# Kernel optimization log

Measured on AMD Instinct MI355X. Metric: run time of the kernel, lower is better.

Reference implementation:

```python
import jax, jax.numpy as jnp
import numpy as np

N = 16384      # nodes (radar cells x batched graphs)
H = 128        # n_hidden
N_ENV = 7
N_IN = N_ENV + 2 + 1  # env + coords + density = 10
T_CTX = 24
HORIZON = 40
T = T_CTX + HORIZON


def setup_inputs() -> dict:
    key = jax.random.key(0)
    ks = jax.random.split(key, 40)

    def w(k, shape, fan_in):
        return jax.random.normal(k, shape, jnp.float32) * np.float32(1.0 / np.sqrt(fan_in))

    inp = {}
    inp["x"] = jax.random.normal(ks[0], (N, T), jnp.float32)
    inp["coords"] = jax.random.normal(ks[1], (N, 2), jnp.float32)
    inp["env"] = jax.random.normal(ks[2], (N, N_ENV, T), jnp.float32)
    # --- encoder params ---
    inp["enc_W_in"] = w(ks[3], (H, N_IN), N_IN)           # Linear(n_in->H), no bias
    inp["enc_Wih0"] = w(ks[4], (4 * H, H), H)
    inp["enc_Whh0"] = w(ks[5], (4 * H, H), H)
    inp["enc_bih0"] = jnp.zeros((4 * H,), jnp.float32)
    inp["enc_bhh0"] = jnp.zeros((4 * H,), jnp.float32)
    inp["enc_Wih1"] = w(ks[6], (4 * H, H), H)
    inp["enc_Whh1"] = w(ks[7], (4 * H, H), H)
    inp["enc_bih1"] = jnp.zeros((4 * H,), jnp.float32)
    inp["enc_bhh1"] = jnp.zeros((4 * H,), jnp.float32)
    # --- NodeLSTM params ---
    inp["node_W_in"] = w(ks[8], (H, N_IN), N_IN)          # Linear(n_in->H), no bias
    inp["in_Wih"] = w(ks[9], (4 * H, 2 * H), 2 * H)       # lstm_in takes [inputs, enc_state]
    inp["in_Whh"] = w(ks[10], (4 * H, H), H)
    inp["in_bih"] = jnp.zeros((4 * H,), jnp.float32)
    inp["in_bhh"] = jnp.zeros((4 * H,), jnp.float32)
    inp["l1_Wih"] = w(ks[11], (4 * H, H), H)
    inp["l1_Whh"] = w(ks[12], (4 * H, H), H)
    inp["l1_bih"] = jnp.zeros((4 * H,), jnp.float32)
    inp["l1_bhh"] = jnp.zeros((4 * H,), jnp.float32)
    # hidden2in / hidden2out heads: Linear(H,H) -> ReLU -> Linear(H,1)
    inp["h2in_W1"] = w(ks[13], (H, H), H)
    inp["h2in_b1"] = jnp.zeros((H,), jnp.float32)
    inp["h2in_W2"] = w(ks[14], (1, H), H)
    inp["h2in_b2"] = jnp.zeros((1,), jnp.float32)
    inp["h2out_W1"] = w(ks[15], (H, H), H)
    inp["h2out_b1"] = jnp.zeros((H,), jnp.float32)
    inp["h2out_W2"] = w(ks[16], (1, H), H)
    inp["h2out_b2"] = jnp.zeros((1,), jnp.float32)
    return inp


def _lstm_cell(xin, h, c, Wih, Whh, bih, bhh):
    # torch.nn.LSTMCell semantics; gate order i, f, g, o
    gates = xin @ Wih.T + h @ Whh.T + (bih + bhh)
    i, f, g, o = jnp.split(gates, 4, axis=1)
    c_new = jax.nn.sigmoid(f) * c + jax.nn.sigmoid(i) * jnp.tanh(g)
    h_new = jax.nn.sigmoid(o) * jnp.tanh(c_new)
    return h_new, c_new


def reference(x, coords, env,
              enc_W_in, enc_Wih0, enc_Whh0, enc_bih0, enc_bhh0,
              enc_Wih1, enc_Whh1, enc_bih1, enc_bhh1,
              node_W_in, in_Wih, in_Whh, in_bih, in_bhh,
              l1_Wih, l1_Whh, l1_bih, l1_bhh,
              h2in_W1, h2in_b1, h2in_W2, h2in_b2,
              h2out_W1, h2out_b1, h2out_W2, h2out_b2):
    n = x.shape[0]
    z = jnp.zeros((n, H), x.dtype)

    # ---------- encoder: scan over T_CTX context steps ----------
    def enc_step(carry, xs):
        h0, c0, h1, c1 = carry
        xt, et = xs  # [N], [N, N_ENV]
        inp = jnp.concatenate([xt[:, None], coords, et], axis=1) @ enc_W_in.T
        h0, c0 = _lstm_cell(inp, h0, c0, enc_Wih0, enc_Whh0, enc_bih0, enc_bhh0)
        h1, c1 = _lstm_cell(h0, h1, c1, enc_Wih1, enc_Whh1, enc_bih1, enc_bhh1)
        return (h0, c0, h1, c1), None

    enc_xs = (x[:, :T_CTX].T, jnp.moveaxis(env[:, :, :T_CTX], 2, 0))
    (h0, c0, h1, c1), _ = jax.lax.scan(enc_step, (z, z, z, z), enc_xs)
    enc_state = h1  # h[-1] captured at setup_states, fixed over the horizon

    def head(hid, W1, b1, W2, b2):
        return jax.nn.sigmoid(jax.nn.relu(hid @ W1.T + b1) @ W2.T + b2)

    # ---------- decoder: scan over HORIZON forecast steps ----------
    def dec_step(carry, et):
        xc, h0, c0, h1, c1 = carry
        inp = jnp.concatenate([xc, coords, et], axis=1) @ node_W_in.T
        inp = jnp.concatenate([inp, enc_state], axis=1)  # [N, 2H]
        h0, c0 = _lstm_cell(inp, h0, c0, in_Wih, in_Whh, in_bih, in_bhh)
        h1, c1 = _lstm_cell(h0, h1, c1, l1_Wih, l1_Whh, l1_bih, l1_bhh)
        x_in = head(h1, h2in_W1, h2in_b1, h2in_W2, h2in_b2)
        x_out = head(h1, h2out_W1, h2out_b1, h2out_W2, h2out_b2)
        xn = xc + x_in - x_out * xc  # source/sink update, [N, 1]
        return (xn, h0, c0, h1, c1), xn

    x0 = x[:, T_CTX - 1][:, None]
    dec_xs = jnp.moveaxis(env[:, :, T_CTX:T_CTX + HORIZON], 2, 0)
    _, ys = jax.lax.scan(dec_step, (x0, h0, c0, h1, c1), dec_xs)  # [HORIZON, N, 1]
    return jnp.transpose(ys[..., 0], (1, 0))  # [N, HORIZON]
```

## Files before the change

kernel.cpp:

```cpp
#include <hip/hip_runtime.h>
#include <hip/hip_bf16.h>
#include <cstdint>
#include <cstddef>

typedef __bf16 bf16_t;
typedef bf16_t bf16x8 __attribute__((ext_vector_type(8)));
typedef bf16_t bf16x4 __attribute__((ext_vector_type(4)));
typedef float  f32x4  __attribute__((ext_vector_type(4)));

#define TT    64
#define T_CTX 24
#define HOR   40
#define ST    136
#define NTH   512

#define MFMA __builtin_amdgcn_mfma_f32_16x16x32_bf16

#define O_WIH0   16
#define O_WHH0   (O_WIH0  + 65536)
#define O_WIH1   (O_WHH0  + 65536)
#define O_WHH1   (O_WIH1  + 65536)
#define O_INWIH  (O_WHH1  + 65536)
#define O_INWHH  (O_INWIH + 131072)
#define O_L1WIH  (O_INWHH + 65536)
#define O_L1WHH  (O_L1WIH + 65536)
#define O_HIW1   (O_L1WHH + 65536)
#define O_HOW1   (O_HIW1  + 16384)
#define O_BIAS   (O_HOW1  + 16384)
#define O_HEADP  (O_BIAS  + 2048)
#define O_WINE   (O_HEADP + 512)
#define O_WINN   (O_WINE  + 1536)
#define O_B2     (O_WINN  + 1536)

struct Ptrs { const void* q[29]; };

__device__ __forceinline__ float sigm(float x) {
  return __builtin_amdgcn_rcpf(1.f + __expf(-x));
}
__device__ __forceinline__ float tanh_(float x) {
  return 1.f - 2.f * __builtin_amdgcn_rcpf(1.f + __expf(2.f * x));
}
__device__ __forceinline__ unsigned pk2(float a, float b) {
  unsigned ua = __float_as_uint(a), ub = __float_as_uint(b);
  ua = (ua + 0x7fffu + ((ua >> 16) & 1u)) >> 16;
  ub = (ub + 0x7fffu + ((ub >> 16) & 1u)) >> 16;
  return ua | (ub << 16);
}
__device__ __forceinline__ float uplo(unsigned p){ return __uint_as_float(p << 16); }
__device__ __forceinline__ float uphi(unsigned p){ return __uint_as_float(p & 0xffff0000u); }

__global__ void detect_kernel(const unsigned short* __restrict__ wsrc, int* __restrict__ flag)
{
  int tid = threadIdx.x;
  int wild = 0;
  for (int i = tid; i < 256; i += 64) {
    unsigned short b = wsrc[i];
    float v  = __uint_as_float(((unsigned)b) << 16);
    float av = fabsf(v);
    unsigned e = (b >> 7) & 0xff;
    if (av > 1000.f || e == 0xff || (((b & 0x7fff) != 0) && av < 1e-9f)) wild++;
  }
  for (int off = 32; off; off >>= 1) wild += __shfl_down(wild, off, 64);
  if (tid == 0) flag[0] = (wild > 16) ? 1 : 0;
}

__global__ void prep_kernel(Ptrs P, bf16_t* __restrict__ w, const int* __restrict__ flag)
{
  const bool f32 = (flag[0] != 0);
  const int gtid = blockIdx.x * blockDim.x + threadIdx.x;
  const int gsz  = gridDim.x * blockDim.x;

  auto rd = [&](const void* src, int i) -> float {
    return f32 ? ((const float*)src)[i] : (float)((const bf16_t*)src)[i];
  };
  auto cp = [&](const void* src, int dst, int n) {
    if (f32) { const float*  s = (const float*)src;
      for (int i = gtid; i < n; i += gsz) w[dst + i] = (bf16_t)s[i];
    } else   { const bf16_t* s = (const bf16_t*)src;
      for (int i = gtid; i < n; i += gsz) w[dst + i] = s[i];
    }
  };

  cp(P.q[4],  O_WIH0,  65536);
  cp(P.q[5],  O_WHH0,  65536);
  cp(P.q[8],  O_WIH1,  65536);
  cp(P.q[9],  O_WHH1,  65536);
  cp(P.q[13], O_INWIH, 131072);
  cp(P.q[14], O_INWHH, 65536);
  cp(P.q[17], O_L1WIH, 65536);
  cp(P.q[18], O_L1WHH, 65536);
  cp(P.q[21], O_HIW1,  16384);
  cp(P.q[25], O_HOW1,  16384);

  for (int i = gtid; i < 512; i += gsz) {
    w[O_BIAS + i]        = (bf16_t)(rd(P.q[6],  i) + rd(P.q[7],  i));
    w[O_BIAS + 512 + i]  = (bf16_t)(rd(P.q[10], i) + rd(P.q[11], i));
    w[O_BIAS + 1024 + i] = (bf16_t)(rd(P.q[15], i) + rd(P.q[16], i));
    w[O_BIAS + 1536 + i] = (bf16_t)(rd(P.q[19], i) + rd(P.q[20], i));
  }
  for (int i = gtid; i < 128; i += gsz) {
    w[O_HEADP + i]       = (bf16_t)rd(P.q[22], i);
    w[O_HEADP + 128 + i] = (bf16_t)rd(P.q[23], i);
    w[O_HEADP + 256 + i] = (bf16_t)rd(P.q[26], i);
    w[O_HEADP + 384 + i] = (bf16_t)rd(P.q[27], i);
  }
  for (int i = gtid; i < 1536; i += gsz) {
    int cc = i / 12, j = i % 12;
    w[O_WINE + i] = (j < 10) ? (bf16_t)rd(P.q[3],  cc * 10 + j) : (bf16_t)0.f;
    w[O_WINN + i] = (j < 10) ? (bf16_t)rd(P.q[12], cc * 10 + j) : (bf16_t)0.f;
  }
  if (gtid == 0) {
    w[O_B2]     = (bf16_t)rd(P.q[24], 0);
    w[O_B2 + 1] = (bf16_t)rd(P.q[28], 0);
  }
}

template<int NKT>
__device__ __forceinline__ void gemm_bt(f32x4 (&acc)[4][4], const bf16_t* __restrict__ As,
                                        const bf16_t* __restrict__ W, int rs, int kofs,
                                        int wid, int l, int q)
{
#pragma unroll
  for (int kt = 0; kt < NKT; ++kt) {
    const int k0 = kt * 32 + q * 8;
    bf16x8 a0 = *(const bf16x8*)(As + (0 * 16 + l) * ST + k0);
    bf16x8 a1 = *(const bf16x8*)(As + (1 * 16 + l) * ST + k0);
    bf16x8 a2 = *(const bf16x8*)(As + (2 * 16 + l) * ST + k0);
    bf16x8 a3 = *(const bf16x8*)(As + (3 * 16 + l) * ST + k0);
#pragma unroll
    for (int g = 0; g < 4; ++g) {
      bf16x8 b = *(const bf16x8*)(W + (size_t)(g * 128 + wid * 16 + l) * rs + kofs + k0);
      acc[g][0] = MFMA(a0, b, acc[g][0], 0, 0, 0);
      acc[g][1] = MFMA(a1, b, acc[g][1], 0, 0, 0);
      acc[g][2] = MFMA(a2, b, acc[g][2], 0, 0, 0);
      acc[g][3] = MFMA(a3, b, acc[g][3], 0, 0, 0);
    }
  }
}

__device__ __forceinline__ void cell_update(f32x4 (&acc)[4][4], float (&c)[16],
                                            bf16_t* __restrict__ sh,
                                            const bf16_t* __restrict__ bias,
                                            int wid, int l, int q)
{
  const int jc = wid * 16 + l;
  const float bi  = (float)bias[jc];
  const float bf_ = (float)bias[128 + jc];
  const float bg  = (float)bias[256 + jc];
  const float bo  = (float)bias[384 + jc];
#pragma unroll
  for (int mt = 0; mt < 4; ++mt) {
#pragma unroll
    for (int r = 0; r < 4; ++r) {
      float gi = acc[0][mt][r] + bi;
      float gf = acc[1][mt][r] + bf_;
      float gg = acc[2][mt][r] + bg;
      float go = acc[3][mt][r] + bo;
      float cn = sigm(gf) * c[mt * 4 + r] + sigm(gi) * tanh_(gg);
      float hh = sigm(go) * tanh_(cn);
      c[mt * 4 + r] = cn;
      sh[(mt * 16 + q * 4 + r) * ST + jc] = (bf16_t)hh;
    }
  }
}

__device__ __forceinline__ void proj16(const float* v, const bf16_t* __restrict__ wbase,
                                       bf16_t* __restrict__ sx, int nd, int sub)
{
  bf16x8 o0, o1;
#pragma unroll
  for (int cc = 0; cc < 16; ++cc) {
    const bf16_t* wr = wbase + (sub * 16 + cc) * 12;
    bf16x4 w0 = *(const bf16x4*)(wr);
    bf16x4 w1 = *(const bf16x4*)(wr + 4);
    bf16x4 w2 = *(const bf16x4*)(wr + 8);
    float a = v[0] * (float)w0[0] + v[1] * (float)w0[1] + v[2] * (float)w0[2] + v[3] * (float)w0[3]
            + v[4] * (float)w1[0] + v[5] * (float)w1[1] + v[6] * (float)w1[2] + v[7] * (float)w1[3]
            + v[8] * (float)w2[0] + v[9] * (float)w2[1];
    if (cc < 8) o0[cc] = (bf16_t)a; else o1[cc - 8] = (bf16_t)a;
  }
  *(bf16x8*)(sx + nd * ST + sub * 16)     = o0;
  *(bf16x8*)(sx + nd * ST + sub * 16 + 8) = o1;
}

template<typename T>
__global__ __launch_bounds__(NTH, 2) void lstm_persist(
    const T* __restrict__ x, const T* __restrict__ coords, const T* __restrict__ env,
    const bf16_t* __restrict__ w, const int* __restrict__ flag, T* __restrict__ out)
{
  const bool want_f32 = (sizeof(T) == 4);
  if ((flag[0] != 0) != want_f32) return;

  __shared__ __align__(16) bf16_t s_x [64 * ST];
  __shared__ __align__(16) bf16_t s_h0[64 * ST];
  __shared__ __align__(16) bf16_t s_h1[64 * ST];
  __shared__ __align__(16) bf16_t s_win[2 * 128 * 12];
  __shared__ __align__(16) bf16_t s_bias[4 * 512];
  __shared__ float s_red[128];
  __shared__ float s_xc[64];

  const int tid = threadIdx.x;
  const int wid = tid >> 6;
  const int l   = tid & 15;
  const int q   = (tid & 63) >> 4;
  const int node0 = blockIdx.x * 64;
  const int nd  = tid >> 3;
  const int sub = tid & 7;

  for (int i = tid; i < 2048; i += NTH) s_bias[i] = w[O_BIAS + i];
  for (int i = tid; i < 3072; i += NTH) s_win[i]  = w[O_WINE + i];
  for (int i = tid; i < 64 * ST; i += NTH) { s_h0[i] = (bf16_t)0.f; s_h1[i] = (bf16_t)0.f; }

  const float cx = (float)coords[(size_t)(node0 + nd) * 2 + 0];
  const float cy = (float)coords[(size_t)(node0 + nd) * 2 + 1];

  float c0[16], c1[16];
#pragma unroll
  for (int i = 0; i < 16; ++i) { c0[i] = 0.f; c1[i] = 0.f; }

  __syncthreads();

#pragma unroll 1
  for (int t = 0; t < T_CTX; ++t) {
    float v[10];
    v[0] = (float)x[(size_t)(node0 + nd) * TT + t];
    v[1] = cx; v[2] = cy;
#pragma unroll
    for (int e = 0; e < 7; ++e)
      v[3 + e] = (float)env[((size_t)(node0 + nd) * 7 + e) * TT + t];
    proj16(v, s_win, s_x, nd, sub);
    __syncthreads();

    f32x4 acc[4][4];
#pragma unroll
    for (int g = 0; g < 4; ++g)
#pragma unroll
      for (int mt = 0; mt < 4; ++mt) acc[g][mt] = f32x4{0.f, 0.f, 0.f, 0.f};
    gemm_bt<4>(acc, s_x,  w + O_WIH0, 128, 0, wid, l, q);
    gemm_bt<4>(acc, s_h0, w + O_WHH0, 128, 0, wid, l, q);
    __syncthreads();
    cell_update(acc, c0, s_h0, s_bias, wid, l, q);
    __syncthreads();

#pragma unroll
    for (int g = 0; g < 4; ++g)
#pragma unroll
      for (int mt = 0; mt < 4; ++mt) acc[g][mt] = f32x4{0.f, 0.f, 0.f, 0.f};
    gemm_bt<4>(acc, s_h0, w + O_WIH1, 128, 0, wid, l, q);
    gemm_bt<4>(acc, s_h1, w + O_WHH1, 128, 0, wid, l, q);
    __syncthreads();
    cell_update(acc, c1, s_h1, s_bias + 512, wid, l, q);
  }
  __syncthreads();

  uint2 geh[4][4], gel[4][4];
  {
    f32x4 acc[4][4];
#pragma unroll
    for (int g = 0; g < 4; ++g)
#pragma unroll
      for (int mt = 0; mt < 4; ++mt) acc[g][mt] = f32x4{0.f, 0.f, 0.f, 0.f};
    gemm_bt<4>(acc, s_h1, w + O_INWIH, 256, 128, wid, l, q);
#pragma unroll
    for (int g = 0; g < 4; ++g)
#pragma unroll
      for (int mt = 0; mt < 4; ++mt) {
        unsigned hx = pk2(acc[g][mt][0], acc[g][mt][1]);
        unsigned hy = pk2(acc[g][mt][2], acc[g][mt][3]);
        geh[g][mt] = uint2{hx, hy};
        gel[g][mt] = uint2{pk2(acc[g][mt][0] - uplo(hx), acc[g][mt][1] - uphi(hx)),
                           pk2(acc[g][mt][2] - uplo(hy), acc[g][mt][3] - uphi(hy))};
      }
  }
  if (tid < 64) s_xc[tid] = (float)x[(size_t)(node0 + tid) * TT + (T_CTX - 1)];
  const float b2i = (float)w[O_B2];
  const float b2o = (float)w[O_B2 + 1];
  const float b1i = (float)w[O_HEADP + wid * 16 + l];
  const float w2i = (float)w[O_HEADP + 128 + wid * 16 + l];
  const float b1o = (float)w[O_HEADP + 256 + wid * 16 + l];
  const float w2o = (float)w[O_HEADP + 384 + wid * 16 + l];
  __syncthreads();

#pragma unroll 1
  for (int s = 0; s < HOR; ++s) {
    const int t = T_CTX + s;
    float v[10];
    v[0] = s_xc[nd];
    v[1] = cx; v[2] = cy;
#pragma unroll
    for (int e = 0; e < 7; ++e)
      v[3 + e] = (float)env[((size_t)(node0 + nd) * 7 + e) * TT + t];
    proj16(v, s_win + 1536, s_x, nd, sub);
    __syncthreads();

    f32x4 acc[4][4];
#pragma unroll
    for (int g = 0; g < 4; ++g)
#pragma unroll
      for (int mt = 0; mt < 4; ++mt)
        acc[g][mt] = f32x4{uplo(geh[g][mt].x) + uplo(gel[g][mt].x),
                           uphi(geh[g][mt].x) + uphi(gel[g][mt].x),
                           uplo(geh[g][mt].y) + uplo(gel[g][mt].y),
                           uphi(geh[g][mt].y) + uphi(gel[g][mt].y)};
    gemm_bt<4>(acc, s_x,  w + O_INWIH, 256, 0, wid, l, q);
    gemm_bt<4>(acc, s_h0, w + O_INWHH, 128, 0, wid, l, q);
    __syncthreads();
    cell_update(acc, c0, s_h0, s_bias + 1024, wid, l, q);
    __syncthreads();

#pragma unroll
    for (int g = 0; g < 4; ++g)
#pragma unroll
      for (int mt = 0; mt < 4; ++mt) acc[g][mt] = f32x4{0.f, 0.f, 0.f, 0.f};
    gemm_bt<4>(acc, s_h0, w + O_L1WIH, 128, 0, wid, l, q);
    gemm_bt<4>(acc, s_h1, w + O_L1WHH, 128, 0, wid, l, q);
    __syncthreads();
    cell_update(acc, c1, s_h1, s_bias + 1536, wid, l, q);
    if (tid < 128) s_red[tid] = 0.f;
    __syncthreads();

    f32x4 hacc[2][4];
#pragma unroll
    for (int hd = 0; hd < 2; ++hd)
#pragma unroll
      for (int mt = 0; mt < 4; ++mt) hacc[hd][mt] = f32x4{0.f, 0.f, 0.f, 0.f};
#pragma unroll
    for (int kt = 0; kt < 4; ++kt) {
      const int k0 = kt * 32 + q * 8;
      bf16x8 a0 = *(const bf16x8*)(s_h1 + (0 * 16 + l) * ST + k0);
      bf16x8 a1 = *(const bf16x8*)(s_h1 + (1 * 16 + l) * ST + k0);
      bf16x8 a2 = *(const bf16x8*)(s_h1 + (2 * 16 + l) * ST + k0);
      bf16x8 a3 = *(const bf16x8*)(s_h1 + (3 * 16 + l) * ST + k0);
      bf16x8 bi_ = *(const bf16x8*)(w + O_HIW1 + (size_t)(wid * 16 + l) * 128 + k0);
      bf16x8 bo_ = *(const bf16x8*)(w + O_HOW1 + (size_t)(wid * 16 + l) * 128 + k0);
      hacc[0][0] = MFMA(a0, bi_, hacc[0][0], 0, 0, 0);
      hacc[0][1] = MFMA(a1, bi_, hacc[0][1], 0, 0, 0);
      hacc[0][2] = MFMA(a2, bi_, hacc[0][2], 0, 0, 0);
      hacc[0][3] = MFMA(a3, bi_, hacc[0][3], 0, 0, 0);
      hacc[1][0] = MFMA(a0, bo_, hacc[1][0], 0, 0, 0);
      hacc[1][1] = MFMA(a1, bo_, hacc[1][1], 0, 0, 0);
      hacc[1][2] = MFMA(a2, bo_, hacc[1][2], 0, 0, 0);
      hacc[1][3] = MFMA(a3, bo_, hacc[1][3], 0, 0, 0);
    }
#pragma unroll
    for (int hd = 0; hd < 2; ++hd) {
      const float b1v = hd ? b1o : b1i;
      const float w2v = hd ? w2o : w2i;
#pragma unroll
      for (int mt = 0; mt < 4; ++mt)
#pragma unroll
        for (int r = 0; r < 4; ++r) {
          float val = fmaxf(hacc[hd][mt][r] + b1v, 0.f) * w2v;
          val += __shfl_xor(val, 1, 64);
          val += __shfl_xor(val, 2, 64);
          val += __shfl_xor(val, 4, 64);
          val += __shfl_xor(val, 8, 64);
          if (l == 0) atomicAdd(&s_red[hd * 64 + mt * 16 + q * 4 + r], val);
        }
    }
    __syncthreads();
    if (tid < 64) {
      float xc = s_xc[tid];
      float si = sigm(s_red[tid] + b2i);
      float so = sigm(s_red[64 + tid] + b2o);
      float xn = xc + si - so * xc;
      s_xc[tid] = xn;
      out[(size_t)(node0 + tid) * HOR + s] = (T)xn;
    }
    __syncthreads();
  }
}

extern "C" void kernel_launch(void* const* d_in, const int* in_sizes, int n_in,
                              void* d_out, int out_size, void* d_ws, size_t ws_size,
                              hipStream_t stream) {
  (void)in_sizes; (void)n_in; (void)out_size; (void)ws_size;
  Ptrs P;
  for (int i = 0; i < 29; ++i) P.q[i] = d_in[i];
  int*    flag = (int*)d_ws;
  bf16_t* w    = (bf16_t*)d_ws;

  detect_kernel<<<1, 64, 0, stream>>>((const unsigned short*)d_in[4], flag);
  prep_kernel<<<256, 256, 0, stream>>>(P, w, flag);
  lstm_persist<float><<<256, NTH, 0, stream>>>(
      (const float*)d_in[0], (const float*)d_in[1], (const float*)d_in[2],
      w, flag, (float*)d_out);
  lstm_persist<bf16_t><<<256, NTH, 0, stream>>>(
      (const bf16_t*)d_in[0], (const bf16_t*)d_in[1], (const bf16_t*)d_in[2],
      w, flag, (bf16_t*)d_out);
}
```

Baseline: 2.216 ms.

## Pre-pack LSTM weights into MFMA fragment order and fuse input/hidden GEMMs

Weights are repacked in the prep kernel into per-wave, per-lane MFMA B-fragment order, so each lane reads a contiguous 16-byte chunk instead of strided rows. Activations [x|h] are now stored side by side in a 256-wide shared buffer, so each LSTM gate GEMM becomes one K=256 pass. The first B fragments of the next GEMM are prefetched before the barrier, and B loads within a GEMM use a three-slot rotating buffer. The constant encoder-state projection is now kept in a single bf16 copy instead of a hi/lo split, which gives up some precision in exchange for fewer registers. Register pressure goes up because of the prefetched fragments.

```diff
diff --git a/kernel.cpp b/kernel.cpp
--- a/kernel.cpp
+++ b/kernel.cpp
@@ -11,26 +11,19 @@
 #define TT    64
 #define T_CTX 24
 #define HOR   40
-#define ST    136
+#define SA    264
 #define NTH   512
 
 #define MFMA __builtin_amdgcn_mfma_f32_16x16x32_bf16
 
-#define O_WIH0   16
-#define O_WHH0   (O_WIH0  + 65536)
-#define O_WIH1   (O_WHH0  + 65536)
-#define O_WHH1   (O_WIH1  + 65536)
-#define O_INWIH  (O_WHH1  + 65536)
-#define O_INWHH  (O_INWIH + 131072)
-#define O_L1WIH  (O_INWHH + 65536)
-#define O_L1WHH  (O_L1WIH + 65536)
-#define O_HIW1   (O_L1WHH + 65536)
-#define O_HOW1   (O_HIW1  + 16384)
-#define O_BIAS   (O_HOW1  + 16384)
-#define O_HEADP  (O_BIAS  + 2048)
-#define O_WINE   (O_HEADP + 512)
-#define O_WINN   (O_WINE  + 1536)
-#define O_B2     (O_WINN  + 1536)
+#define O_PKE   16
+#define O_PKD   (O_PKE + 262144)
+#define O_PKX   (O_PKD + 294912)
+#define O_BIAS  (O_PKX + 131072)
+#define O_HEADP (O_BIAS + 2048)
+#define O_WINE  (O_HEADP + 512)
+#define O_WINN  (O_WINE + 1536)
+#define O_B2    (O_WINN + 1536)
 
 struct Ptrs { const void* q[29]; };
 
@@ -64,84 +57,123 @@
   if (tid == 0) flag[0] = (wild > 16) ? 1 : 0;
 }
 
-__global__ void prep_kernel(Ptrs P, bf16_t* __restrict__ w, const int* __restrict__ flag)
+__global__ void prep_kernel(Ptrs P, bf16_t* __restrict__ wb, const int* __restrict__ flag)
 {
   const bool f32 = (flag[0] != 0);
   const int gtid = blockIdx.x * blockDim.x + threadIdx.x;
   const int gsz  = gridDim.x * blockDim.x;
-
   auto rd = [&](const void* src, int i) -> float {
     return f32 ? ((const float*)src)[i] : (float)((const bf16_t*)src)[i];
   };
-  auto cp = [&](const void* src, int dst, int n) {
-    if (f32) { const float*  s = (const float*)src;
-      for (int i = gtid; i < n; i += gsz) w[dst + i] = (bf16_t)s[i];
-    } else   { const bf16_t* s = (const bf16_t*)src;
-      for (int i = gtid; i < n; i += gsz) w[dst + i] = s[i];
-    }
-  };
-
-  cp(P.q[4],  O_WIH0,  65536);
-  cp(P.q[5],  O_WHH0,  65536);
-  cp(P.q[8],  O_WIH1,  65536);
-  cp(P.q[9],  O_WHH1,  65536);
-  cp(P.q[13], O_INWIH, 131072);
-  cp(P.q[14], O_INWHH, 65536);
-  cp(P.q[17], O_L1WIH, 65536);
-  cp(P.q[18], O_L1WHH, 65536);
-  cp(P.q[21], O_HIW1,  16384);
-  cp(P.q[25], O_HOW1,  16384);
-
+
+  for (int i = gtid; i < 262144; i += gsz) {
+    int w = i >> 15, r = i & 32767, f = r >> 9, e = r & 511;
+    int ln = e >> 3, j = e & 7;
+    int seg = f >> 5, fk = f & 31, kt = fk >> 2, g = fk & 3;
+    int row = g * 128 + w * 16 + (ln & 15);
+    int col = kt * 32 + ((ln >> 4) << 3) + j;
+    float v;
+    if (seg == 0) v = (col < 128) ? rd(P.q[4], row * 128 + col) : rd(P.q[5], row * 128 + col - 128);
+    else          v = (col < 128) ? rd(P.q[8], row * 128 + col) : rd(P.q[9], row * 128 + col - 128);
+    wb[O_PKE + i] = (bf16_t)v;
+  }
+  for (int i = gtid; i < 294912; i += gsz) {
+    int w = i / 36864, r = i - w * 36864, f = r >> 9, e = r & 511;
+    int ln = e >> 3, j = e & 7;
+    int colk = ((ln >> 4) << 3) + j;
+    float v;
+    if (f < 64) {
+      int seg = f >> 5, fk = f & 31, kt = fk >> 2, g = fk & 3;
+      int row = g * 128 + w * 16 + (ln & 15);
+      int col = kt * 32 + colk;
+      if (seg == 0) v = (col < 128) ? rd(P.q[13], row * 256 + col) : rd(P.q[14], row * 128 + col - 128);
+      else          v = (col < 128) ? rd(P.q[17], row * 128 + col) : rd(P.q[18], row * 128 + col - 128);
+    } else {
+      int f2 = f - 64, h = f2 >> 2, kt = f2 & 3;
+      int row = w * 16 + (ln & 15);
+      int col = kt * 32 + colk;
+      v = rd(h ? P.q[25] : P.q[21], row * 128 + col);
+    }
+    wb[O_PKD + i] = (bf16_t)v;
+  }
+  for (int i = gtid; i < 131072; i += gsz) {
+    int w = i >> 14, r = i & 16383, f = r >> 9, e = r & 511;
+    int ln = e >> 3, j = e & 7;
+    int kt = f >> 2, g = f & 3;
+    int row = g * 128 + w * 16 + (ln & 15);
+    int col = kt * 32 + ((ln >> 4) << 3) + j;
+    wb[O_PKX + i] = (bf16_t)rd(P.q[13], row * 256 + 128 + col);
+  }
   for (int i = gtid; i < 512; i += gsz) {
-    w[O_BIAS + i]        = (bf16_t)(rd(P.q[6],  i) + rd(P.q[7],  i));
-    w[O_BIAS + 512 + i]  = (bf16_t)(rd(P.q[10], i) + rd(P.q[11], i));
-    w[O_BIAS + 1024 + i] = (bf16_t)(rd(P.q[15], i) + rd(P.q[16], i));
-    w[O_BIAS + 1536 + i] = (bf16_t)(rd(P.q[19], i) + rd(P.q[20], i));
+    wb[O_BIAS + i]        = (bf16_t)(rd(P.q[6],  i) + rd(P.q[7],  i));
+    wb[O_BIAS + 512 + i]  = (bf16_t)(rd(P.q[10], i) + rd(P.q[11], i));
+    wb[O_BIAS + 1024 + i] = (bf16_t)(rd(P.q[15], i) + rd(P.q[16], i));
+    wb[O_BIAS + 1536 + i] = (bf16_t)(rd(P.q[19], i) + rd(P.q[20], i));
   }
   for (int i = gtid; i < 128; i += gsz) {
-    w[O_HEADP + i]       = (bf16_t)rd(P.q[22], i);
-    w[O_HEADP + 128 + i] = (bf16_t)rd(P.q[23], i);
-    w[O_HEADP + 256 + i] = (bf16_t)rd(P.q[26], i);
-    w[O_HEADP + 384 + i] = (bf16_t)rd(P.q[27], i);
+    wb[O_HEADP + i]       = (bf16_t)rd(P.q[22], i);
+    wb[O_HEADP + 128 + i] = (bf16_t)rd(P.q[23], i);
+    wb[O_HEADP + 256 + i] = (bf16_t)rd(P.q[26], i);
+    wb[O_HEADP + 384 + i] = (bf16_t)rd(P.q[27], i);
   }
   for (int i = gtid; i < 1536; i += gsz) {
     int cc = i / 12, j = i % 12;
-    w[O_WINE + i] = (j < 10) ? (bf16_t)rd(P.q[3],  cc * 10 + j) : (bf16_t)0.f;
-    w[O_WINN + i] = (j < 10) ? (bf16_t)rd(P.q[12], cc * 10 + j) : (bf16_t)0.f;
+    wb[O_WINE + i] = (j < 10) ? (bf16_t)rd(P.q[3],  cc * 10 + j) : (bf16_t)0.f;
+    wb[O_WINN + i] = (j < 10) ? (bf16_t)rd(P.q[12], cc * 10 + j) : (bf16_t)0.f;
   }
   if (gtid == 0) {
-    w[O_B2]     = (bf16_t)rd(P.q[24], 0);
-    w[O_B2 + 1] = (bf16_t)rd(P.q[28], 0);
-  }
+    wb[O_B2]     = (bf16_t)rd(P.q[24], 0);
+    wb[O_B2 + 1] = (bf16_t)rd(P.q[28], 0);
+  }
+}
+
+struct PreB { bf16x8 b[2][4]; };
+
+__device__ __forceinline__ PreB preB(const bf16_t* __restrict__ pl) {
+  PreB r;
+#pragma unroll
+  for (int p = 0; p < 2; ++p)
+#pragma unroll
+    for (int g = 0; g < 4; ++g)
+      r.b[p][g] = *(const bf16x8*)(pl + (p * 4 + g) * 512);
+  return r;
 }
 
 template<int NKT>
-__device__ __forceinline__ void gemm_bt(f32x4 (&acc)[4][4], const bf16_t* __restrict__ As,
-                                        const bf16_t* __restrict__ W, int rs, int kofs,
+__device__ __forceinline__ void gemm_pk(f32x4 (&acc)[4][4], const bf16_t* __restrict__ As,
+                                        const bf16_t* __restrict__ pl, const PreB& pre,
+                                        int l, int q)
+{
+  bf16x8 bw[3][4];
+#pragma unroll
+  for (int g = 0; g < 4; ++g) { bw[0][g] = pre.b[0][g]; bw[1][g] = pre.b[1][g]; }
+#pragma unroll
+  for (int kt = 0; kt < NKT; ++kt) {
+    bf16x8 a[4];
+#pragma unroll
+    for (int mt = 0; mt < 4; ++mt)
+      a[mt] = *(const bf16x8*)(As + (mt * 16 + l) * SA + kt * 32 + q * 8);
+    if (kt + 2 < NKT) {
+#pragma unroll
+      for (int g = 0; g < 4; ++g)
+        bw[(kt + 2) % 3][g] = *(const bf16x8*)(pl + ((kt + 2) * 4 + g) * 512);
+    }
+#pragma unroll
+    for (int g = 0; g < 4; ++g) {
+      bf16x8 b = bw[kt % 3][g];
+      acc[g][0] = MFMA(a[0], b, acc[g][0], 0, 0, 0);
+      acc[g][1] = MFMA(a[1], b, acc[g][1], 0, 0, 0);
+      acc[g][2] = MFMA(a[2], b, acc[g][2], 0, 0, 0);
+      acc[g][3] = MFMA(a[3], b, acc[g][3], 0, 0, 0);
+    }
+  }
+}
+
+template<bool DUAL>
+__device__ __forceinline__ void cell_up(f32x4 (&acc)[4][4], float (&c)[16],
+                                        bf16_t* __restrict__ shb, bf16_t* __restrict__ sha,
+                                        const bf16_t* __restrict__ bias,
                                         int wid, int l, int q)
-{
-#pragma unroll
-  for (int kt = 0; kt < NKT; ++kt) {
-    const int k0 = kt * 32 + q * 8;
-    bf16x8 a0 = *(const bf16x8*)(As + (0 * 16 + l) * ST + k0);
-    bf16x8 a1 = *(const bf16x8*)(As + (1 * 16 + l) * ST + k0);
-    bf16x8 a2 = *(const bf16x8*)(As + (2 * 16 + l) * ST + k0);
-    bf16x8 a3 = *(const bf16x8*)(As + (3 * 16 + l) * ST + k0);
-#pragma unroll
-    for (int g = 0; g < 4; ++g) {
-      bf16x8 b = *(const bf16x8*)(W + (size_t)(g * 128 + wid * 16 + l) * rs + kofs + k0);
-      acc[g][0] = MFMA(a0, b, acc[g][0], 0, 0, 0);
-      acc[g][1] = MFMA(a1, b, acc[g][1], 0, 0, 0);
-      acc[g][2] = MFMA(a2, b, acc[g][2], 0, 0, 0);
-      acc[g][3] = MFMA(a3, b, acc[g][3], 0, 0, 0);
-    }
-  }
-}
-
-__device__ __forceinline__ void cell_update(f32x4 (&acc)[4][4], float (&c)[16],
-                                            bf16_t* __restrict__ sh,
-                                            const bf16_t* __restrict__ bias,
-                                            int wid, int l, int q)
 {
   const int jc = wid * 16 + l;
   const float bi  = (float)bias[jc];
@@ -159,7 +191,9 @@
       float cn = sigm(gf) * c[mt * 4 + r] + sigm(gi) * tanh_(gg);
       float hh = sigm(go) * tanh_(cn);
       c[mt * 4 + r] = cn;
-      sh[(mt * 16 + q * 4 + r) * ST + jc] = (bf16_t)hh;
+      const int row = mt * 16 + q * 4 + r;
+      shb[row * SA + jc] = (bf16_t)hh;
+      if (DUAL) sha[row * SA + jc] = (bf16_t)hh;
     }
   }
 }
@@ -179,8 +213,8 @@
             + v[8] * (float)w2[0] + v[9] * (float)w2[1];
     if (cc < 8) o0[cc] = (bf16_t)a; else o1[cc - 8] = (bf16_t)a;
   }
-  *(bf16x8*)(sx + nd * ST + sub * 16)     = o0;
-  *(bf16x8*)(sx + nd * ST + sub * 16 + 8) = o1;
+  *(bf16x8*)(sx + nd * SA + sub * 16)     = o0;
+  *(bf16x8*)(sx + nd * SA + sub * 16 + 8) = o1;
 }
 
 template<typename T>
@@ -191,25 +225,32 @@
   const bool want_f32 = (sizeof(T) == 4);
   if ((flag[0] != 0) != want_f32) return;
 
-  __shared__ __align__(16) bf16_t s_x [64 * ST];
-  __shared__ __align__(16) bf16_t s_h0[64 * ST];
-  __shared__ __align__(16) bf16_t s_h1[64 * ST];
+  __shared__ __align__(16) bf16_t bufA[64 * SA];
+  __shared__ __align__(16) bf16_t bufB[64 * SA];
   __shared__ __align__(16) bf16_t s_win[2 * 128 * 12];
   __shared__ __align__(16) bf16_t s_bias[4 * 512];
   __shared__ float s_red[128];
   __shared__ float s_xc[64];
 
-  const int tid = threadIdx.x;
-  const int wid = tid >> 6;
-  const int l   = tid & 15;
-  const int q   = (tid & 63) >> 4;
+  const int tid  = threadIdx.x;
+  const int wid  = tid >> 6;
+  const int lane = tid & 63;
+  const int l    = tid & 15;
+  const int q    = (tid & 63) >> 4;
   const int node0 = blockIdx.x * 64;
   const int nd  = tid >> 3;
   const int sub = tid & 7;
 
+  const bf16_t* plE0 = w + O_PKE + wid * 32768 + lane * 8;
+  const bf16_t* plE1 = plE0 + 16384;
+  const bf16_t* plD0 = w + O_PKD + wid * 36864 + lane * 8;
+  const bf16_t* plD1 = plD0 + 16384;
+  const bf16_t* plH  = plD0 + 32768;
+  const bf16_t* plX  = w + O_PKX + wid * 16384 + lane * 8;
+
   for (int i = tid; i < 2048; i += NTH) s_bias[i] = w[O_BIAS + i];
   for (int i = tid; i < 3072; i += NTH) s_win[i]  = w[O_WINE + i];
-  for (int i = tid; i < 64 * ST; i += NTH) { s_h0[i] = (bf16_t)0.f; s_h1[i] = (bf16_t)0.f; }
+  for (int i = tid; i < 64 * SA; i += NTH) { bufA[i] = (bf16_t)0.f; bufB[i] = (bf16_t)0.f; }
 
   const float cx = (float)coords[(size_t)(node0 + nd) * 2 + 0];
   const float cy = (float)coords[(size_t)(node0 + nd) * 2 + 1];
@@ -218,6 +259,7 @@
 #pragma unroll
   for (int i = 0; i < 16; ++i) { c0[i] = 0.f; c1[i] = 0.f; }
 
+  PreB pA = preB(plE0);
   __syncthreads();
 
 #pragma unroll 1
@@ -228,7 +270,7 @@
 #pragma unroll
     for (int e = 0; e < 7; ++e)
       v[3 + e] = (float)env[((size_t)(node0 + nd) * 7 + e) * TT + t];
-    proj16(v, s_win, s_x, nd, sub);
+    proj16(v, s_win, bufA, nd, sub);
     __syncthreads();
 
     f32x4 acc[4][4];
@@ -236,41 +278,37 @@
     for (int g = 0; g < 4; ++g)
 #pragma unroll
       for (int mt = 0; mt < 4; ++mt) acc[g][mt] = f32x4{0.f, 0.f, 0.f, 0.f};
-    gemm_bt<4>(acc, s_x,  w + O_WIH0, 128, 0, wid, l, q);
-    gemm_bt<4>(acc, s_h0, w + O_WHH0, 128, 0, wid, l, q);
-    __syncthreads();
-    cell_update(acc, c0, s_h0, s_bias, wid, l, q);
+    gemm_pk<8>(acc, bufA, plE0, pA, l, q);
+    PreB pC = preB(plE1);
+    __syncthreads();
+    cell_up<true>(acc, c0, bufB, bufA + 128, s_bias, wid, l, q);
     __syncthreads();
 
 #pragma unroll
     for (int g = 0; g < 4; ++g)
 #pragma unroll
       for (int mt = 0; mt < 4; ++mt) acc[g][mt] = f32x4{0.f, 0.f, 0.f, 0.f};
-    gemm_bt<4>(acc, s_h0, w + O_WIH1, 128, 0, wid, l, q);
-    gemm_bt<4>(acc, s_h1, w + O_WHH1, 128, 0, wid, l, q);
-    __syncthreads();
-    cell_update(acc, c1, s_h1, s_bias + 512, wid, l, q);
+    gemm_pk<8>(acc, bufB, plE1, pC, l, q);
+    pA = preB((t < T_CTX - 1) ? plE0 : plX);
+    __syncthreads();
+    cell_up<false>(acc, c1, bufB + 128, nullptr, s_bias + 512, wid, l, q);
   }
   __syncthreads();
 
-  uint2 geh[4][4], gel[4][4];
+  uint2 geh[4][4];
   {
     f32x4 acc[4][4];
 #pragma unroll
     for (int g = 0; g < 4; ++g)
 #pragma unroll
       for (int mt = 0; mt < 4; ++mt) acc[g][mt] = f32x4{0.f, 0.f, 0.f, 0.f};
-    gemm_bt<4>(acc, s_h1, w + O_INWIH, 256, 128, wid, l, q);
-#pragma unroll
-    for (int g = 0; g < 4; ++g)
-#pragma unroll
-      for (int mt = 0; mt < 4; ++mt) {
-        unsigned hx = pk2(acc[g][mt][0], acc[g][mt][1]);
-        unsigned hy = pk2(acc[g][mt][2], acc[g][mt][3]);
-        geh[g][mt] = uint2{hx, hy};
-        gel[g][mt] = uint2{pk2(acc[g][mt][0] - uplo(hx), acc[g][mt][1] - uphi(hx)),
-                           pk2(acc[g][mt][2] - uplo(hy), acc[g][mt][3] - uphi(hy))};
-      }
+    gemm_pk<4>(acc, bufB + 128, plX, pA, l, q);
+#pragma unroll
+    for (int g = 0; g < 4; ++g)
+#pragma unroll
+      for (int mt = 0; mt < 4; ++mt)
+        geh[g][mt] = uint2{pk2(acc[g][mt][0], acc[g][mt][1]),
+                           pk2(acc[g][mt][2], acc[g][mt][3])};
   }
   if (tid < 64) s_xc[tid] = (float)x[(size_t)(node0 + tid) * TT + (T_CTX - 1)];
   const float b2i = (float)w[O_B2];
@@ -279,6 +317,7 @@
   const float w2i = (float)w[O_HEADP + 128 + wid * 16 + l];
   const float b1o = (float)w[O_HEADP + 256 + wid * 16 + l];
   const float w2o = (float)w[O_HEADP + 384 + wid * 16 + l];
+  pA = preB(plD0);
   __syncthreads();
 
 #pragma unroll 1
@@ -290,7 +329,7 @@
 #pragma unroll
     for (int e = 0; e < 7; ++e)
       v[3 + e] = (float)env[((size_t)(node0 + nd) * 7 + e) * TT + t];
-    proj16(v, s_win + 1536, s_x, nd, sub);
+    proj16(v, s_win + 1536, bufA, nd, sub);
     __syncthreads();
 
     f32x4 acc[4][4];
@@ -298,25 +337,26 @@
     for (int g = 0; g < 4; ++g)
 #pragma unroll
       for (int mt = 0; mt < 4; ++mt)
-        acc[g][mt] = f32x4{uplo(geh[g][mt].x) + uplo(gel[g][mt].x),
-                           uphi(geh[g][mt].x) + uphi(gel[g][mt].x),
-                           uplo(geh[g][mt].y) + uplo(gel[g][mt].y),
-                           uphi(geh[g][mt].y) + uphi(gel[g][mt].y)};
-    gemm_bt<4>(acc, s_x,  w + O_INWIH, 256, 0, wid, l, q);
-    gemm_bt<4>(acc, s_h0, w + O_INWHH, 128, 0, wid, l, q);
-    __syncthreads();
-    cell_update(acc, c0, s_h0, s_bias + 1024, wid, l, q);
+        acc[g][mt] = f32x4{uplo(geh[g][mt].x), uphi(geh[g][mt].x),
+                           uplo(geh[g][mt].y), uphi(geh[g][mt].y)};
+    gemm_pk<8>(acc, bufA, plD0, pA, l, q);
+    PreB pC = preB(plD1);
+    __syncthreads();
+    cell_up<true>(acc, c0, bufB, bufA + 128, s_bias + 1024, wid, l, q);
     __syncthreads();
 
 #pragma unroll
     for (int g = 0; g < 4; ++g)
 #pragma unroll
       for (int mt = 0; mt < 4; ++mt) acc[g][mt] = f32x4{0.f, 0.f, 0.f, 0.f};
-    gemm_bt<4>(acc, s_h0, w + O_L1WIH, 128, 0, wid, l, q);
-    gemm_bt<4>(acc, s_h1, w + O_L1WHH, 128, 0, wid, l, q);
-    __syncthreads();
-    cell_update(acc, c1, s_h1, s_bias + 1536, wid, l, q);
+    gemm_pk<8>(acc, bufB, plD1, pC, l, q);
+    bf16x8 hb[8];
+#pragma unroll
+    for (int f = 0; f < 8; ++f) hb[f] = *(const bf16x8*)(plH + f * 512);
+    __syncthreads();
+    cell_up<false>(acc, c1, bufB + 128, nullptr, s_bias + 1536, wid, l, q);
     if (tid < 128) s_red[tid] = 0.f;
+    pA = preB(plD0);
     __syncthreads();
 
     f32x4 hacc[2][4];
@@ -326,21 +366,15 @@
       for (int mt = 0; mt < 4; ++mt) hacc[hd][mt] = f32x4{0.f, 0.f, 0.f, 0.f};
 #pragma unroll
     for (int kt = 0; kt < 4; ++kt) {
-      const int k0 = kt * 32 + q * 8;
-      bf16x8 a0 = *(const bf16x8*)(s_h1 + (0 * 16 + l) * ST + k0);
-      bf16x8 a1 = *(const bf16x8*)(s_h1 + (1 * 16 + l) * ST + k0);
-      bf16x8 a2 = *(const bf16x8*)(s_h1 + (2 * 16 + l) * ST + k0);
-      bf16x8 a3 = *(const bf16x8*)(s_h1 + (3 * 16 + l) * ST + k0);
-      bf16x8 bi_ = *(const bf16x8*)(w + O_HIW1 + (size_t)(wid * 16 + l) * 128 + k0);
-      bf16x8 bo_ = *(const bf16x8*)(w + O_HOW1 + (size_t)(wid * 16 + l) * 128 + k0);
-      hacc[0][0] = MFMA(a0, bi_, hacc[0][0], 0, 0, 0);
-      hacc[0][1] = MFMA(a1, bi_, hacc[0][1], 0, 0, 0);
-      hacc[0][2] = MFMA(a2, bi_, hacc[0][2], 0, 0, 0);
-      hacc[0][3] = MFMA(a3, bi_, hacc[0][3], 0, 0, 0);
-      hacc[1][0] = MFMA(a0, bo_, hacc[1][0], 0, 0, 0);
-      hacc[1][1] = MFMA(a1, bo_, hacc[1][1], 0, 0, 0);
-      hacc[1][2] = MFMA(a2, bo_, hacc[1][2], 0, 0, 0);
-      hacc[1][3] = MFMA(a3, bo_, hacc[1][3], 0, 0, 0);
+      bf16x8 a[4];
+#pragma unroll
+      for (int mt = 0; mt < 4; ++mt)
+        a[mt] = *(const bf16x8*)(bufB + 128 + (mt * 16 + l) * SA + kt * 32 + q * 8);
+#pragma unroll
+      for (int mt = 0; mt < 4; ++mt) {
+        hacc[0][mt] = MFMA(a[mt], hb[kt],     hacc[0][mt], 0, 0, 0);
+        hacc[1][mt] = MFMA(a[mt], hb[4 + kt], hacc[1][mt], 0, 0, 0);
+      }
     }
 #pragma unroll
     for (int hd = 0; hd < 2; ++hd) {
```

New measurement: 2.159 ms. 2.5% less time.
